# Kernel optimization log

Measured on AMD Instinct MI355X. Metric: run time of the kernel, lower is better.

Reference implementation:

```python
import jax, jax.numpy as jnp
import numpy as np

V, C, D = 131072, 64, 8


def setup_inputs() -> dict:
    key = jax.random.key(0)
    kx, kw = jax.random.split(key)
    x = jax.random.normal(kx, (V, C * D), dtype=jnp.float32)
    # Stacked per-channel Linear weights: W[c] has torch layout (out, in) = (D, D).
    # (Original init is identity; random weights exercise the same math.)
    W = jax.random.normal(kw, (C, D, D), dtype=jnp.float32)
    return {"x": x, "W": W}


def reference(x, W):
    # x: (V, C*D) -> (V, D, C) as in torch reshape(x.shape[0], D, -1)
    c, d = W.shape[0], W.shape[1]
    xr = x.reshape(x.shape[0], d, c)
    # Ox[v, e, j] = sum_d xr[v, d, j] * W[j, e, d]   (torch Linear: y = x @ W.T)
    # einsum 'bki,bkj->bi' contracts k AND sums over j of Ox, so precompute
    # s[v, k] = sum_j Ox[v, k, j] in one fused contraction:
    s = jnp.einsum('vdc,ckd->vk', xr, W)          # (V, D)
    xOx = jnp.einsum('vk,vki->vi', s, xr)         # (V, C)
    return jnp.tanh(xOx)
```

## Files before the change

### kernel.cpp

```cpp
#include <hip/hip_runtime.h>
#include <hip/hip_bf16.h>


__device__ __forceinline__ float fast_tanh(float x) {
    float e = __expf(2.0f * x);
    return 1.0f - 2.0f / (e + 1.0f);
}

__global__ __launch_bounds__(256, 4)
void ipf_kernel(const float* __restrict__ x, const float* __restrict__ W,
                float* __restrict__ out, int V) {
    const int tid   = blockIdx.x * blockDim.x + threadIdx.x;
    const int lane  = threadIdx.x & 63;
    const int wave  = tid >> 6;
    const int nwav  = (gridDim.x * blockDim.x) >> 6;

    const int d0 = lane >> 4;
    const int c0 = (lane & 15) << 2;

    float Wa[4][8], Wb[4][8];
#pragma unroll
    for (int j = 0; j < 4; ++j) {
        const float* wp = W + (size_t)(c0 + j) * 64 + d0;
#pragma unroll
        for (int k = 0; k < 8; ++k) {
            Wa[j][k] = wp[k * 8];
            Wb[j][k] = wp[k * 8 + 4];
        }
    }

    const float4* __restrict__ x4   = reinterpret_cast<const float4*>(x);
    float4* __restrict__       out4 = reinterpret_cast<float4*>(out);

    for (int v = wave; v < V; v += nwav) {
        const float4 a = x4[(size_t)v * 128 + lane];
        const float4 b = x4[(size_t)v * 128 + 64 + lane];
        const float xa[4] = {a.x, a.y, a.z, a.w};
        const float xb[4] = {b.x, b.y, b.z, b.w};

        float p[8];
#pragma unroll
        for (int k = 0; k < 8; ++k) {
            float acc = 0.0f;
#pragma unroll
            for (int j = 0; j < 4; ++j) {
                acc = fmaf(xa[j], Wa[j][k], acc);
                acc = fmaf(xb[j], Wb[j][k], acc);
            }
            p[k] = acc;
        }

#pragma unroll
        for (int k = 0; k < 8; ++k) {
            p[k] += __shfl_xor(p[k], 16, 64);
            p[k] += __shfl_xor(p[k], 32, 64);
        }

        float u = (d0 & 2) ? ((d0 & 1) ? p[3] : p[2]) : ((d0 & 1) ? p[1] : p[0]);
        float w = (d0 & 2) ? ((d0 & 1) ? p[7] : p[6]) : ((d0 & 1) ? p[5] : p[4]);
#pragma unroll
        for (int m = 1; m <= 8; m <<= 1) {
            u += __shfl_xor(u, m, 64);
            w += __shfl_xor(w, m, 64);
        }

        float q0 = fmaf(u, xa[0], w * xb[0]);
        float q1 = fmaf(u, xa[1], w * xb[1]);
        float q2 = fmaf(u, xa[2], w * xb[2]);
        float q3 = fmaf(u, xa[3], w * xb[3]);
        q0 += __shfl_xor(q0, 16, 64); q0 += __shfl_xor(q0, 32, 64);
        q1 += __shfl_xor(q1, 16, 64); q1 += __shfl_xor(q1, 32, 64);
        q2 += __shfl_xor(q2, 16, 64); q2 += __shfl_xor(q2, 32, 64);
        q3 += __shfl_xor(q3, 16, 64); q3 += __shfl_xor(q3, 32, 64);

        if (lane < 16) {
            float4 o;
            o.x = fast_tanh(q0);
            o.y = fast_tanh(q1);
            o.z = fast_tanh(q2);
            o.w = fast_tanh(q3);
            out4[(size_t)v * 16 + lane] = o;
        }
    }
}

extern "C" void kernel_launch(void* const* d_in, const int* in_sizes, int n_in,
                              void* d_out, int out_size, void* d_ws, size_t ws_size,
                              hipStream_t stream) {
    const float* x = (const float*)d_in[0];
    const float* W = (const float*)d_in[1];
    float* out = (float*)d_out;
    const int V = in_sizes[0] / 512;

    const int block = 256;
    const int grid  = 2048;
    ipf_kernel<<<grid, block, 0, stream>>>(x, W, out, V);
}
```

Baseline: 100.4 us.

## Prefetch next row, use DPP row reductions and fold-based butterfly transposes

Loads the next row's x values before computing the current one, so global-memory latency overlaps with the arithmetic. Replaces the 16-lane cross-lane sums with DPP row reductions. Uses paired fold shuffles that halve the number of cross-lane exchanges in both the reduction and the output stage. The output is now written as one scalar per lane, with all 64 lanes active, instead of float4 writes from 16 lanes. The cost is extra register pressure from the prefetched values and scalar (non-vector) stores.

```diff
diff --git a/kernel.cpp b/kernel.cpp
--- a/kernel.cpp
+++ b/kernel.cpp
@@ -7,13 +7,42 @@
     return 1.0f - 2.0f / (e + 1.0f);
 }
 
+__device__ __forceinline__ float fold16(float a, float b, int lane) {
+    float x   = (lane & 16) ? a : b;
+    float sh  = __shfl_xor(x, 16, 64);
+    float own = (lane & 16) ? b : a;
+    return own + sh;
+}
+
+__device__ __forceinline__ float fold32(float a, float b, int lane) {
+    float x   = (lane & 32) ? a : b;
+    float sh  = __shfl_xor(x, 32, 64);
+    float own = (lane & 32) ? b : a;
+    return own + sh;
+}
+
+template <int CTRL>
+__device__ __forceinline__ float dpp_add(float v) {
+    int i = __builtin_bit_cast(int, v);
+    int p = __builtin_amdgcn_update_dpp(i, i, CTRL, 0xF, 0xF, false);
+    return v + __builtin_bit_cast(float, p);
+}
+
+__device__ __forceinline__ float row16_sum(float v) {
+    v = dpp_add<0xB1>(v);
+    v = dpp_add<0x4E>(v);
+    v = dpp_add<0x141>(v);
+    v = dpp_add<0x140>(v);
+    return v;
+}
+
 __global__ __launch_bounds__(256, 4)
 void ipf_kernel(const float* __restrict__ x, const float* __restrict__ W,
                 float* __restrict__ out, int V) {
-    const int tid   = blockIdx.x * blockDim.x + threadIdx.x;
-    const int lane  = threadIdx.x & 63;
-    const int wave  = tid >> 6;
-    const int nwav  = (gridDim.x * blockDim.x) >> 6;
+    const int tid  = blockIdx.x * blockDim.x + threadIdx.x;
+    const int lane = threadIdx.x & 63;
+    const int wave = tid >> 6;
+    const int nwav = (gridDim.x * blockDim.x) >> 6;
 
     const int d0 = lane >> 4;
     const int c0 = (lane & 15) << 2;
@@ -29,12 +58,22 @@
         }
     }
 
-    const float4* __restrict__ x4   = reinterpret_cast<const float4*>(x);
-    float4* __restrict__       out4 = reinterpret_cast<float4*>(out);
+    const float4* __restrict__ x4 = reinterpret_cast<const float4*>(x);
 
-    for (int v = wave; v < V; v += nwav) {
-        const float4 a = x4[(size_t)v * 128 + lane];
-        const float4 b = x4[(size_t)v * 128 + 64 + lane];
+    int v = wave;
+    if (v >= V) return;
+    float4 a = x4[(size_t)v * 128 + lane];
+    float4 b = x4[(size_t)v * 128 + 64 + lane];
+
+    while (true) {
+        const int vn = v + nwav;
+        const bool more = (vn < V);
+        float4 an = a, bn = b;
+        if (more) {
+            an = x4[(size_t)vn * 128 + lane];
+            bn = x4[(size_t)vn * 128 + 64 + lane];
+        }
+
         const float xa[4] = {a.x, a.y, a.z, a.w};
         const float xb[4] = {b.x, b.y, b.z, b.w};
 
@@ -51,36 +90,29 @@
         }
 
 #pragma unroll
-        for (int k = 0; k < 8; ++k) {
-            p[k] += __shfl_xor(p[k], 16, 64);
-            p[k] += __shfl_xor(p[k], 32, 64);
-        }
+        for (int k = 0; k < 8; ++k) p[k] = row16_sum(p[k]);
 
-        float u = (d0 & 2) ? ((d0 & 1) ? p[3] : p[2]) : ((d0 & 1) ? p[1] : p[0]);
-        float w = (d0 & 2) ? ((d0 & 1) ? p[7] : p[6]) : ((d0 & 1) ? p[5] : p[4]);
-#pragma unroll
-        for (int m = 1; m <= 8; m <<= 1) {
-            u += __shfl_xor(u, m, 64);
-            w += __shfl_xor(w, m, 64);
-        }
+        float t0 = fold16(p[0], p[1], lane);
+        float t1 = fold16(p[2], p[3], lane);
+        float t2 = fold16(p[4], p[5], lane);
+        float t3 = fold16(p[6], p[7], lane);
+        float u = fold32(t0, t1, lane);
+        float w = fold32(t2, t3, lane);
 
         float q0 = fmaf(u, xa[0], w * xb[0]);
         float q1 = fmaf(u, xa[1], w * xb[1]);
         float q2 = fmaf(u, xa[2], w * xb[2]);
         float q3 = fmaf(u, xa[3], w * xb[3]);
-        q0 += __shfl_xor(q0, 16, 64); q0 += __shfl_xor(q0, 32, 64);
-        q1 += __shfl_xor(q1, 16, 64); q1 += __shfl_xor(q1, 32, 64);
-        q2 += __shfl_xor(q2, 16, 64); q2 += __shfl_xor(q2, 32, 64);
-        q3 += __shfl_xor(q3, 16, 64); q3 += __shfl_xor(q3, 32, 64);
 
-        if (lane < 16) {
-            float4 o;
-            o.x = fast_tanh(q0);
-            o.y = fast_tanh(q1);
-            o.z = fast_tanh(q2);
-            o.w = fast_tanh(q3);
-            out4[(size_t)v * 16 + lane] = o;
-        }
+        float A = fold16(q0, q1, lane);
+        float B = fold16(q2, q3, lane);
+        float r = fold32(A, B, lane);
+
+        const int col = ((lane & 15) << 2) + d0;
+        out[(size_t)v * 64 + col] = fast_tanh(r);
+
+        if (!more) break;
+        v = vn; a = an; b = bn;
     }
 }
 
```

Measured after the change: 92.22 us. -8.2%, faster.
